# Kernel tuning notes

Measured on AMD Instinct MI355X. Metric: run time of the kernel, lower is better.

Reference implementation:

```python
import jax, jax.numpy as jnp
import numpy as np

B, L, H = 512, 1000, 128  # batch, time steps, hidden size


def setup_inputs() -> dict:
    key = jax.random.key(0)
    ks = jax.random.split(key, 12)
    s = 1.0 / np.sqrt(H)

    def u(k, shape):
        return jax.random.uniform(k, shape, jnp.float32, -s, s)

    return {
        "y": jax.random.normal(ks[0], (B, L), jnp.float32),
        # LSTMCell 1: input size 1 -> H (torch gate order i, f, g, o)
        "W_ih1": u(ks[1], (4 * H, 1)),
        "W_hh1": u(ks[2], (4 * H, H)),
        "b_ih1": u(ks[3], (4 * H,)),
        "b_hh1": u(ks[4], (4 * H,)),
        # LSTMCell 2: H -> H
        "W_ih2": u(ks[5], (4 * H, H)),
        "W_hh2": u(ks[6], (4 * H, H)),
        "b_ih2": u(ks[7], (4 * H,)),
        "b_hh2": u(ks[8], (4 * H,)),
        # Linear H -> 1
        "W_lin": u(ks[9], (1, H)),
        "b_lin": u(ks[10], (1,)),
    }


def _lstm_cell(x, h, c, W_ih, W_hh, b_ih, b_hh):
    # torch.nn.LSTMCell: gates = x W_ih^T + b_ih + h W_hh^T + b_hh, order i,f,g,o
    g = x @ W_ih.T + b_ih + h @ W_hh.T + b_hh  # [B, 4H]
    i, f, gg, o = jnp.split(g, 4, axis=-1)
    i = jax.nn.sigmoid(i)
    f = jax.nn.sigmoid(f)
    gg = jnp.tanh(gg)
    o = jax.nn.sigmoid(o)
    c_new = f * c + i * gg
    h_new = o * jnp.tanh(c_new)
    return h_new, c_new


def reference(y, W_ih1, W_hh1, b_ih1, b_hh1, W_ih2, W_hh2, b_ih2, b_hh2, W_lin, b_lin):
    n = y.shape[0]
    z = jnp.zeros((n, H), y.dtype)

    def step(carry, x_t):
        h1, c1, h2, c2 = carry
        x_t = x_t[:, None]  # [B, 1]
        h1, c1 = _lstm_cell(x_t, h1, c1, W_ih1, W_hh1, b_ih1, b_hh1)
        h2, c2 = _lstm_cell(h1, h2, c2, W_ih2, W_hh2, b_ih2, b_hh2)
        out = h2 @ W_lin.T + b_lin  # [B, 1]
        return (h1, c1, h2, c2), out[:, 0]

    _, outs = jax.lax.scan(step, (z, z, z, z), y.T)  # outs: [L, B]
    return outs.T  # [B, L]
```

## Files before the change

### kernel.cpp

```cpp
#include <hip/hip_runtime.h>

typedef _Float16 half2_t __attribute__((ext_vector_type(2)));
typedef _Float16 half8_t __attribute__((ext_vector_type(8)));

union h8pack { half8_t v; half2_t h2[4]; };

constexpr int BATCH = 512;
constexpr int SEQ   = 1000;
constexpr int HID   = 128;
constexpr int GATES = 4 * HID;
constexpr int TPB   = 512;
constexpr int ROWS  = 2;

#if __has_builtin(__builtin_amdgcn_fdot2)
__device__ __forceinline__ float fdot2(half2_t a, half2_t b, float c) {
  return __builtin_amdgcn_fdot2(a, b, c, false);
}
#else
__device__ __forceinline__ float fdot2(half2_t a, half2_t b, float c) {
  return c + (float)a[0] * (float)b[0] + (float)a[1] * (float)b[1];
}
#endif

__device__ __forceinline__ float fast_sigmoid(float x) {
  x = fminf(fmaxf(x, -30.f), 30.f);
  return __fdividef(1.f, 1.f + __expf(-x));
}
__device__ __forceinline__ float fast_tanh(float x) {
  x = fminf(fmaxf(x, -15.f), 15.f);
  float e = __expf(2.f * x);
  return __fdividef(e - 1.f, e + 1.f);
}

__global__ __launch_bounds__(TPB, 2)
void lstm_persist(const float* __restrict__ y,
                  const float* __restrict__ W_ih1,
                  const float* __restrict__ W_hh1,
                  const float* __restrict__ b_ih1,
                  const float* __restrict__ b_hh1,
                  const float* __restrict__ W_ih2,
                  const float* __restrict__ W_hh2,
                  const float* __restrict__ b_ih2,
                  const float* __restrict__ b_hh2,
                  const float* __restrict__ W_lin,
                  const float* __restrict__ b_lin,
                  float* __restrict__ out)
{
  const int tid = threadIdx.x;
  const int j   = tid;
  const int r0  = blockIdx.x * ROWS;

  __shared__ alignas(16) half8_t h1_sh[ROWS][HID / 8];
  __shared__ alignas(16) half8_t h2_sh[ROWS][HID / 8];
  __shared__ float g1_sh[ROWS][GATES];
  __shared__ float g2_sh[ROWS][GATES];
  __shared__ float red_sh[4];

  half2_t w1[HID / 2], w2[HID / 2], w3[HID / 2];
  {
    const float2* p1 = (const float2*)(W_hh1 + (size_t)j * HID);
    const float2* p2 = (const float2*)(W_ih2 + (size_t)j * HID);
    const float2* p3 = (const float2*)(W_hh2 + (size_t)j * HID);
#pragma unroll
    for (int k = 0; k < HID / 2; ++k) {
      float2 a  = p1[k]; w1[k] = half2_t{(_Float16)a.x,  (_Float16)a.y};
      float2 bb = p2[k]; w2[k] = half2_t{(_Float16)bb.x, (_Float16)bb.y};
      float2 cc = p3[k]; w3[k] = half2_t{(_Float16)cc.x, (_Float16)cc.y};
    }
  }
  const float wih1  = W_ih1[j];
  const float bias1 = b_ih1[j] + b_hh1[j];
  const float bias2 = b_ih2[j] + b_hh2[j];
  const float wlin  = W_lin[tid & (HID - 1)];
  const float blin  = b_lin[0];

  if (tid < 64) {
    half8_t z = {};
    if (tid < 32) ((half8_t*)h1_sh)[tid] = z;
    else          ((half8_t*)h2_sh)[tid - 32] = z;
  }
  __syncthreads();

  const float* xr0 = y + (size_t)r0 * SEQ;
  const float* xr1 = xr0 + SEQ;
  float c1v = 0.f, c2v = 0.f;

  for (int t = 0; t < SEQ; ++t) {
    float x0 = xr0[t], x1 = xr1[t];
    float a0 = fmaf(x0, wih1, bias1);
    float a1 = fmaf(x1, wih1, bias1);
#pragma unroll
    for (int c = 0; c < HID / 8; ++c) {
      h8pack u0, u1;
      u0.v = h1_sh[0][c];
      u1.v = h1_sh[1][c];
#pragma unroll
      for (int q = 0; q < 4; ++q) {
        a0 = fdot2(w1[4 * c + q], u0.h2[q], a0);
        a1 = fdot2(w1[4 * c + q], u1.h2[q], a1);
      }
    }
    g1_sh[0][j] = a0;
    g1_sh[1][j] = a1;
    __syncthreads();

    if (tid < ROWS * HID) {
      const int r = tid >> 7, jj = tid & (HID - 1);
      float gi = g1_sh[r][jj];
      float gf = g1_sh[r][jj + HID];
      float gg = g1_sh[r][jj + 2 * HID];
      float go = g1_sh[r][jj + 3 * HID];
      float iv = fast_sigmoid(gi);
      float fv = fast_sigmoid(gf);
      float gv = fast_tanh(gg);
      float ov = fast_sigmoid(go);
      c1v = fmaf(fv, c1v, iv * gv);
      float h = ov * fast_tanh(c1v);
      ((_Float16*)h1_sh)[tid] = (_Float16)h;
    }
    __syncthreads();

    float s0a = bias2, s1a = bias2, s0b = 0.f, s1b = 0.f;
#pragma unroll
    for (int c = 0; c < HID / 8; ++c) {
      h8pack u0, u1, v0, v1;
      u0.v = h1_sh[0][c];
      u1.v = h1_sh[1][c];
      v0.v = h2_sh[0][c];
      v1.v = h2_sh[1][c];
#pragma unroll
      for (int q = 0; q < 4; ++q) {
        s0a = fdot2(w2[4 * c + q], u0.h2[q], s0a);
        s1a = fdot2(w2[4 * c + q], u1.h2[q], s1a);
        s0b = fdot2(w3[4 * c + q], v0.h2[q], s0b);
        s1b = fdot2(w3[4 * c + q], v1.h2[q], s1b);
      }
    }
    g2_sh[0][j] = s0a + s0b;
    g2_sh[1][j] = s1a + s1b;
    __syncthreads();

    float pred = 0.f;
    if (tid < ROWS * HID) {
      const int r = tid >> 7, jj = tid & (HID - 1);
      float gi = g2_sh[r][jj];
      float gf = g2_sh[r][jj + HID];
      float gg = g2_sh[r][jj + 2 * HID];
      float go = g2_sh[r][jj + 3 * HID];
      float iv = fast_sigmoid(gi);
      float fv = fast_sigmoid(gf);
      float gv = fast_tanh(gg);
      float ov = fast_sigmoid(go);
      c2v = fmaf(fv, c2v, iv * gv);
      float h = ov * fast_tanh(c2v);
      ((_Float16*)h2_sh)[tid] = (_Float16)h;
      pred = h * wlin;
#pragma unroll
      for (int off = 32; off > 0; off >>= 1)
        pred += __shfl_down(pred, off);
      if ((tid & 63) == 0) red_sh[tid >> 6] = pred;
    }
    __syncthreads();
    if (tid < ROWS) {
      out[(size_t)(r0 + tid) * SEQ + t] = red_sh[2 * tid] + red_sh[2 * tid + 1] + blin;
    }
  }
}

extern "C" void kernel_launch(void* const* d_in, const int* in_sizes, int n_in,
                              void* d_out, int out_size, void* d_ws, size_t ws_size,
                              hipStream_t stream) {
  const float* y     = (const float*)d_in[0];
  const float* W_ih1 = (const float*)d_in[1];
  const float* W_hh1 = (const float*)d_in[2];
  const float* b_ih1 = (const float*)d_in[3];
  const float* b_hh1 = (const float*)d_in[4];
  const float* W_ih2 = (const float*)d_in[5];
  const float* W_hh2 = (const float*)d_in[6];
  const float* b_ih2 = (const float*)d_in[7];
  const float* b_hh2 = (const float*)d_in[8];
  const float* W_lin = (const float*)d_in[9];
  const float* b_lin = (const float*)d_in[10];
  float* out = (float*)d_out;

  lstm_persist<<<BATCH / ROWS, TPB, 0, stream>>>(
      y, W_ih1, W_hh1, b_ih1, b_hh1, W_ih2, W_hh2, b_ih2, b_hh2, W_lin, b_lin, out);
}
```

Baseline: 3.001 ms.

## Split gate dot products across thread pairs and drop a per-step barrier

Doubles the block to 1024 threads, with each pair of threads splitting a gate row's K dimension in half and combining the partial sums via shfl_xor. This halves the per-thread dot-product chain and weight register footprint. The input sequence is also preloaded into shared memory, and layer-2 elementwise work moves to two whole waves that write the output directly, removing the fourth barrier per step. The trade-offs are an extra shuffle per reduction, more threads synchronising at each barrier, and lower block occupancy per CU.

```diff
diff --git a/kernel.cpp b/kernel.cpp
--- a/kernel.cpp
+++ b/kernel.cpp
@@ -9,8 +9,9 @@
 constexpr int SEQ   = 1000;
 constexpr int HID   = 128;
 constexpr int GATES = 4 * HID;
-constexpr int TPB   = 512;
+constexpr int TPB   = 1024;
 constexpr int ROWS  = 2;
+constexpr int KHALF = HID / 2;
 
 #if __has_builtin(__builtin_amdgcn_fdot2)
 __device__ __forceinline__ float fdot2(half2_t a, half2_t b, float c) {
@@ -32,7 +33,19 @@
   return __fdividef(e - 1.f, e + 1.f);
 }
 
-__global__ __launch_bounds__(TPB, 2)
+__device__ __forceinline__ void load_half_row(const float* __restrict__ src,
+                                              half2_t* dst) {
+  const float4* p = (const float4*)src;
+#pragma unroll
+  for (int k = 0; k < KHALF / 4; ++k) {
+    float4 f = p[k];
+    dst[2 * k]     = half2_t{(_Float16)f.x, (_Float16)f.y};
+    dst[2 * k + 1] = half2_t{(_Float16)f.z, (_Float16)f.w};
+    if ((k & 3) == 3) asm volatile("" ::: "memory");
+  }
+}
+
+__global__ __launch_bounds__(TPB)
 void lstm_persist(const float* __restrict__ y,
                   const float* __restrict__ W_ih1,
                   const float* __restrict__ W_hh1,
@@ -47,61 +60,65 @@
                   float* __restrict__ out)
 {
   const int tid = threadIdx.x;
-  const int j   = tid;
+  const int j   = tid >> 1;
+  const int kh  = tid & 1;
   const int r0  = blockIdx.x * ROWS;
 
   __shared__ alignas(16) half8_t h1_sh[ROWS][HID / 8];
   __shared__ alignas(16) half8_t h2_sh[ROWS][HID / 8];
   __shared__ float g1_sh[ROWS][GATES];
   __shared__ float g2_sh[ROWS][GATES];
-  __shared__ float red_sh[4];
-
-  half2_t w1[HID / 2], w2[HID / 2], w3[HID / 2];
-  {
-    const float2* p1 = (const float2*)(W_hh1 + (size_t)j * HID);
-    const float2* p2 = (const float2*)(W_ih2 + (size_t)j * HID);
-    const float2* p3 = (const float2*)(W_hh2 + (size_t)j * HID);
-#pragma unroll
-    for (int k = 0; k < HID / 2; ++k) {
-      float2 a  = p1[k]; w1[k] = half2_t{(_Float16)a.x,  (_Float16)a.y};
-      float2 bb = p2[k]; w2[k] = half2_t{(_Float16)bb.x, (_Float16)bb.y};
-      float2 cc = p3[k]; w3[k] = half2_t{(_Float16)cc.x, (_Float16)cc.y};
-    }
-  }
-  const float wih1  = W_ih1[j];
-  const float bias1 = b_ih1[j] + b_hh1[j];
-  const float bias2 = b_ih2[j] + b_hh2[j];
-  const float wlin  = W_lin[tid & (HID - 1)];
-  const float blin  = b_lin[0];
-
+  __shared__ float x_sh[ROWS][SEQ + 8];
+
+  for (int i = tid; i < ROWS * SEQ; i += TPB) {
+    const int r  = (i >= SEQ) ? 1 : 0;
+    const int tt = i - r * SEQ;
+    x_sh[r][tt] = y[(size_t)(r0 + r) * SEQ + tt];
+  }
   if (tid < 64) {
     half8_t z = {};
     if (tid < 32) ((half8_t*)h1_sh)[tid] = z;
     else          ((half8_t*)h2_sh)[tid - 32] = z;
   }
+
+  half2_t w1[KHALF / 2], w2[KHALF / 2], w3[KHALF / 2];
+  load_half_row(W_hh1 + (size_t)j * HID + kh * KHALF, w1);
+  load_half_row(W_ih2 + (size_t)j * HID + kh * KHALF, w2);
+  load_half_row(W_hh2 + (size_t)j * HID + kh * KHALF, w3);
+
+  const float wih1  = W_ih1[j];
+  const float bias1 = b_ih1[j] + b_hh1[j];
+  const float bias2 = b_ih2[j] + b_hh2[j];
+  const float wla   = W_lin[tid & 63];
+  const float wlb   = W_lin[(tid & 63) + 64];
+  const float blin  = b_lin[0];
+
+  float c1v = 0.f;
+  float c2a = 0.f, c2b = 0.f;
+
   __syncthreads();
 
-  const float* xr0 = y + (size_t)r0 * SEQ;
-  const float* xr1 = xr0 + SEQ;
-  float c1v = 0.f, c2v = 0.f;
+  float x0 = x_sh[0][0], x1 = x_sh[1][0];
+  float xn0 = 0.f, xn1 = 0.f;
 
   for (int t = 0; t < SEQ; ++t) {
-    float x0 = xr0[t], x1 = xr1[t];
-    float a0 = fmaf(x0, wih1, bias1);
-    float a1 = fmaf(x1, wih1, bias1);
-#pragma unroll
-    for (int c = 0; c < HID / 8; ++c) {
+    float a0, a1;
+    if (kh == 0) { a0 = fmaf(x0, wih1, bias1); a1 = fmaf(x1, wih1, bias1); }
+    else         { a0 = 0.f;                   a1 = 0.f; }
+#pragma unroll
+    for (int c = 0; c < 8; ++c) {
       h8pack u0, u1;
-      u0.v = h1_sh[0][c];
-      u1.v = h1_sh[1][c];
+      u0.v = h1_sh[0][kh * 8 + c];
+      u1.v = h1_sh[1][kh * 8 + c];
 #pragma unroll
       for (int q = 0; q < 4; ++q) {
         a0 = fdot2(w1[4 * c + q], u0.h2[q], a0);
         a1 = fdot2(w1[4 * c + q], u1.h2[q], a1);
       }
     }
-    g1_sh[0][j] = a0;
-    g1_sh[1][j] = a1;
+    a0 += __shfl_xor(a0, 1);
+    a1 += __shfl_xor(a1, 1);
+    if (kh == 0) { g1_sh[0][j] = a0; g1_sh[1][j] = a1; }
     __syncthreads();
 
     if (tid < ROWS * HID) {
@@ -115,55 +132,68 @@
       float gv = fast_tanh(gg);
       float ov = fast_sigmoid(go);
       c1v = fmaf(fv, c1v, iv * gv);
-      float h = ov * fast_tanh(c1v);
-      ((_Float16*)h1_sh)[tid] = (_Float16)h;
+      ((_Float16*)h1_sh)[tid] = (_Float16)(ov * fast_tanh(c1v));
     }
     __syncthreads();
 
-    float s0a = bias2, s1a = bias2, s0b = 0.f, s1b = 0.f;
-#pragma unroll
-    for (int c = 0; c < HID / 8; ++c) {
-      h8pack u0, u1, v0, v1;
-      u0.v = h1_sh[0][c];
-      u1.v = h1_sh[1][c];
-      v0.v = h2_sh[0][c];
-      v1.v = h2_sh[1][c];
+    float s0, s1;
+    if (kh == 0) { s0 = bias2; s1 = bias2; }
+    else         { s0 = 0.f;   s1 = 0.f; }
+#pragma unroll
+    for (int c = 0; c < 8; ++c) {
+      h8pack u0, u1;
+      u0.v = h1_sh[0][kh * 8 + c];
+      u1.v = h1_sh[1][kh * 8 + c];
 #pragma unroll
       for (int q = 0; q < 4; ++q) {
-        s0a = fdot2(w2[4 * c + q], u0.h2[q], s0a);
-        s1a = fdot2(w2[4 * c + q], u1.h2[q], s1a);
-        s0b = fdot2(w3[4 * c + q], v0.h2[q], s0b);
-        s1b = fdot2(w3[4 * c + q], v1.h2[q], s1b);
+        s0 = fdot2(w2[4 * c + q], u0.h2[q], s0);
+        s1 = fdot2(w2[4 * c + q], u1.h2[q], s1);
       }
     }
-    g2_sh[0][j] = s0a + s0b;
-    g2_sh[1][j] = s1a + s1b;
+    xn0 = x_sh[0][t + 1];
+    xn1 = x_sh[1][t + 1];
+#pragma unroll
+    for (int c = 0; c < 8; ++c) {
+      h8pack v0, v1;
+      v0.v = h2_sh[0][kh * 8 + c];
+      v1.v = h2_sh[1][kh * 8 + c];
+#pragma unroll
+      for (int q = 0; q < 4; ++q) {
+        s0 = fdot2(w3[4 * c + q], v0.h2[q], s0);
+        s1 = fdot2(w3[4 * c + q], v1.h2[q], s1);
+      }
+    }
+    s0 += __shfl_xor(s0, 1);
+    s1 += __shfl_xor(s1, 1);
+    if (kh == 0) { g2_sh[0][j] = s0; g2_sh[1][j] = s1; }
     __syncthreads();
 
-    float pred = 0.f;
-    if (tid < ROWS * HID) {
-      const int r = tid >> 7, jj = tid & (HID - 1);
-      float gi = g2_sh[r][jj];
-      float gf = g2_sh[r][jj + HID];
-      float gg = g2_sh[r][jj + 2 * HID];
-      float go = g2_sh[r][jj + 3 * HID];
-      float iv = fast_sigmoid(gi);
-      float fv = fast_sigmoid(gf);
-      float gv = fast_tanh(gg);
-      float ov = fast_sigmoid(go);
-      c2v = fmaf(fv, c2v, iv * gv);
-      float h = ov * fast_tanh(c2v);
-      ((_Float16*)h2_sh)[tid] = (_Float16)h;
-      pred = h * wlin;
+    const int wv = tid >> 6;
+    if (wv == 4 || wv == 7) {
+      const int r = (wv == 4) ? 0 : 1;
+      const int l = tid & 63;
+      float gia = g2_sh[r][l],       gib = g2_sh[r][l + 64];
+      float gfa = g2_sh[r][l + 128], gfb = g2_sh[r][l + 192];
+      float gga = g2_sh[r][l + 256], ggb = g2_sh[r][l + 320];
+      float goa = g2_sh[r][l + 384], gob = g2_sh[r][l + 448];
+      float iva = fast_sigmoid(gia), ivb = fast_sigmoid(gib);
+      float fva = fast_sigmoid(gfa), fvb = fast_sigmoid(gfb);
+      float gva = fast_tanh(gga),    gvb = fast_tanh(ggb);
+      float ova = fast_sigmoid(goa), ovb = fast_sigmoid(gob);
+      c2a = fmaf(fva, c2a, iva * gva);
+      c2b = fmaf(fvb, c2b, ivb * gvb);
+      float ha = ova * fast_tanh(c2a);
+      float hb = ovb * fast_tanh(c2b);
+      _Float16* hp = (_Float16*)h2_sh;
+      hp[r * HID + l]      = (_Float16)ha;
+      hp[r * HID + l + 64] = (_Float16)hb;
+      float pred = fmaf(ha, wla, hb * wlb);
 #pragma unroll
       for (int off = 32; off > 0; off >>= 1)
         pred += __shfl_down(pred, off);
-      if ((tid & 63) == 0) red_sh[tid >> 6] = pred;
-    }
-    __syncthreads();
-    if (tid < ROWS) {
-      out[(size_t)(r0 + tid) * SEQ + t] = red_sh[2 * tid] + red_sh[2 * tid + 1] + blin;
-    }
+      if (l == 0) out[(size_t)(r0 + r) * SEQ + t] = pred + blin;
+    }
+    x0 = xn0; x1 = xn1;
   }
 }
 
```

Result: slower. 4.576 ms (+52.4%).
